# Optimization experiments

Hardware: AMD Instinct MI355X
Metric: run time of the kernel (lower is better)

## Reference

```python
import jax, jax.numpy as jnp
import numpy as np

K_NN = 8        # neighbors
RADIUS = 0.1    # neighbor distance cutoff


def setup_inputs() -> dict:
    key = jax.random.key(0)
    k1, k2 = jax.random.split(key)
    B, N, KS = 2, 8192, 16  # batch, points, mask slots
    pc = jax.random.uniform(k1, (B, N, 3), dtype=jnp.float32)
    mask = jax.random.uniform(k2, (B, N, KS), dtype=jnp.float32)
    return {"pc": pc, "mask": mask}


def _knn(k, pc):
    # squared pairwise distances via gemm: (B,N,N)
    sq = jnp.sum(pc * pc, axis=-1)
    d2 = sq[:, :, None] + sq[:, None, :] - 2.0 * jnp.einsum("bnd,bmd->bnm", pc, pc)
    d2 = jnp.maximum(d2, 0.0)
    neg_d2, idx = jax.lax.top_k(-d2, k)          # k smallest distances
    dist = jnp.sqrt(jnp.maximum(-neg_d2, 0.0))   # (B,N,k) euclidean
    return dist, idx


def reference(pc, mask):
    # mask: (B,N,KS) -> (B,KS,N)
    mask_t = jnp.transpose(mask, (0, 2, 1))
    dist, idx = _knn(K_NN, pc)                   # (B,N,k) each
    # replace out-of-radius neighbors with the self index (nearest = self)
    self_idx = idx[:, :, :1]                     # (B,N,1)
    idx = jnp.where(dist > RADIUS, self_idx, idx)
    idx = jax.lax.stop_gradient(idx)
    # grouping_operation: (B,KS,N) gathered at (B,N,k) -> (B,KS,N,k)
    nn_mask = jax.vmap(lambda f, i: f[:, i])(mask_t, idx)
    # loss_norm=1: L1 norm over mask-slot dim (dim=1), mean over k, mean overall
    diff = mask_t[:, :, :, None] - nn_mask       # (B,KS,N,k)
    loss = jnp.sum(jnp.abs(diff), axis=1).mean(axis=-1)  # (B,N)
    return loss.mean()
```

## Files before the change

kernel.cpp:

```cpp
#include <hip/hip_runtime.h>

#define BATCH 2
#define NPTS  8192
#define KS    16
#define KNN   8
#define R2LOOSE 0.0101f
#define KEYMASK 0xFFFFE000u
#define NCELL   1000
#define CSTRIDE 1024

#define QB       64
#define NWAVE    8
#define NTHREADS 512
#define CAP      32
#define TILEC    1024
#define NBLK     (BATCH * NPTS / QB)

__device__ __forceinline__ int cell_of(float x, float y, float z) {
    int cx = (int)(x * 10.0f); cx = cx > 9 ? 9 : cx;
    int cy = (int)(y * 10.0f); cy = cy > 9 ? 9 : cy;
    int cz = (int)(z * 10.0f); cz = cz > 9 ? 9 : cz;
    return (cx * 10 + cy) * 10 + cz;
}

__global__ __launch_bounds__(1024) void build_kernel(
    const float* __restrict__ pc,
    float4* __restrict__ cs, int* __restrict__ sidx,
    int* __restrict__ cstart, float* __restrict__ out)
{
    __shared__ int h[1024];
    __shared__ int wsum[16];
    const int blk = blockIdx.x, t = threadIdx.x;
    const int b = blk >> 3, seg = blk & 7;
    const int lane = t & 63, w = t >> 6;

    h[t] = 0;
    if (blk == 0 && t == 0) out[0] = 0.0f;

    const float* p = pc + (size_t)b * NPTS * 3;
    float X[8], Y[8], Z[8]; int CC[8];
#pragma unroll
    for (int j = 0; j < 8; ++j) {
        const int i = j * 1024 + t;
        X[j] = p[3 * i]; Y[j] = p[3 * i + 1]; Z[j] = p[3 * i + 2];
        CC[j] = cell_of(X[j], Y[j], Z[j]);
    }
    __syncthreads();

    int myold = 0;
#pragma unroll
    for (int j = 0; j < 8; ++j) {
        const int old = atomicAdd(&h[CC[j]], 1);
        if (j == seg) myold = old;
        __syncthreads();
    }

    const int sum = h[t];
    int inc = sum;
#pragma unroll
    for (int off = 1; off < 64; off <<= 1) {
        const int v = __shfl_up(inc, off);
        if (lane >= off) inc += v;
    }
    if (lane == 63) wsum[w] = inc;
    __syncthreads();
    if (w == 0) {
        const int v = (lane < 16) ? wsum[lane] : 0;
        int iv = v;
#pragma unroll
        for (int off = 1; off < 16; off <<= 1) {
            const int u = __shfl_up(iv, off);
            if (lane >= off) iv += u;
        }
        if (lane < 16) wsum[lane] = iv - v;
    }
    __syncthreads();
    const int excl = inc - sum + wsum[w];
    if (seg == 0) cstart[b * CSTRIDE + t] = excl;
    __syncthreads();
    h[t] = excl;
    __syncthreads();

    float mx = X[0], my_ = Y[0], mz = Z[0]; int mc = CC[0];
#pragma unroll
    for (int j = 1; j < 8; ++j)
        if (seg == j) { mx = X[j]; my_ = Y[j]; mz = Z[j]; mc = CC[j]; }

    const int pos = h[mc] + myold;
    const float sq = fmaf(mz, mz, fmaf(my_, my_, mx * mx));
    cs[b * NPTS + pos]   = make_float4(mx, my_, mz, -0.5f * sq);
    sidx[b * NPTS + pos] = seg * 1024 + t;
}

__global__ __launch_bounds__(512) void knn_loss_kernel(
    const float4* __restrict__ cs,
    const int*    __restrict__ sidx,
    const int*    __restrict__ cstart,
    const float*  __restrict__ mask,
    float* __restrict__ out)
{
    __shared__ float4   tile[TILEC];
    __shared__ int      tsp[TILEC];
    __shared__ unsigned sbuf[CAP * NTHREADS];
    __shared__ int      fidx[QB * KNN];
    __shared__ int      qid[QB];
    __shared__ float    red[NWAVE];

    const int t = threadIdx.x;
    const int q = t & (QB - 1);
    const int s = t >> 6;
    const int su = __builtin_amdgcn_readfirstlane(s);
    const int blk = blockIdx.x;
    const int b  = blk >> 7;
    const int q0 = (blk & 127) * QB;
    const int qpos = q0 + q;

    const float4* csb = cs + b * NPTS;
    const float4 qc = csb[qpos];
    const int    qi = sidx[b * NPTS + qpos];
    if (s == 0) qid[q] = qi;

    const float qx = qc.x, qy = qc.y, qz = qc.z;
    const float qs = -2.0f * qc.w;
    const float negthr = (qs - R2LOOSE) * 0.5f;
    const unsigned SENT = (__float_as_uint(R2LOOSE) & KEYMASK) | 0x1FFFu;

    int lex = cell_of(qx, qy, qz);
    int cmn = lex, cmx = lex;
#pragma unroll
    for (int off = 32; off; off >>= 1) {
        cmn = min(cmn, __shfl_xor(cmn, off));
        cmx = max(cmx, __shfl_xor(cmx, off));
    }
    const int cfirst = __builtin_amdgcn_readfirstlane(cmn);
    const int clast  = __builtin_amdgcn_readfirstlane(cmx);

    int lo0 = cfirst - 111, h0 = clast - 89;
    int lo1 = cfirst - 11,  h1 = clast + 11;
    int lo2 = cfirst + 89,  h2 = clast + 111;
    lo0 = min(max(lo0, 0), 1000);
    lo1 = min(max(lo1, 0), 1000);
    lo2 = min(max(lo2, 0), 1000);
    int hp0 = min(max(h0 + 1, 0), 1000);
    int hp1 = min(max(h1 + 1, 0), 1000);
    int hp2 = min(max(h2 + 1, 0), 1000);
    lo1 = max(lo1, hp0);
    lo2 = max(lo2, hp1);

    const int* csp = cstart + b * CSTRIDE;
    const int P0 = csp[lo0], E0 = csp[hp0];
    const int P1 = csp[lo1], E1 = csp[hp1];
    const int P2 = csp[lo2], E2 = csp[hp2];
    const int L0 = max(0, E0 - P0);
    const int L1 = max(0, E1 - P1);
    const int L2 = max(0, E2 - P2);
    const int C  = L0 + L1 + L2;

    int cnt = 0;
    auto EVAL = [&](const float4& c, int spos) {
        const float tt = fmaf(c.x, qx, fmaf(c.y, qy, fmaf(c.z, qz, c.w)));
        const float d2 = fmaxf(fmaf(-2.0f, tt, qs), 0.0f);
        const unsigned key =
            (__float_as_uint(d2) & KEYMASK) | (unsigned)spos;
        const int slot = cnt < (CAP - 1) ? cnt : (CAP - 1);
        sbuf[slot * NTHREADS + t] = key;
        cnt += (tt >= negthr) ? 1 : 0;
    };

    for (int tb = 0; tb < C; tb += TILEC) {
        const int nt = min(TILEC, C - tb);
        for (int p = t; p < nt; p += NTHREADS) {
            const int g = tb + p;
            int sp = P0 + g;
            sp = (g >= L0)      ? (P1 + (g - L0))      : sp;
            sp = (g >= L0 + L1) ? (P2 + (g - L0 - L1)) : sp;
            tile[p] = csb[sp];
            tsp[p]  = sp;
        }
        __syncthreads();

        int j = (su * nt) >> 3;
        const int e = ((su + 1) * nt) >> 3;
        for (; j + 4 <= e; j += 4) {
            const float4 c0 = tile[j],     c1 = tile[j + 1];
            const float4 c2 = tile[j + 2], c3 = tile[j + 3];
            const int s0 = tsp[j],     s1 = tsp[j + 1];
            const int s2 = tsp[j + 2], s3 = tsp[j + 3];
            EVAL(c0, s0); EVAL(c1, s1); EVAL(c2, s2); EVAL(c3, s3);
        }
        for (; j < e; ++j) { const float4 c0 = tile[j]; EVAL(c0, tsp[j]); }
        __syncthreads();
    }

    unsigned md[KNN];
#pragma unroll
    for (int k = 0; k < KNN; ++k) md[k] = SENT;
    const int m = cnt < CAP ? cnt : CAP;
    for (int k = 0; k < m; ++k) {
        unsigned ky = sbuf[k * NTHREADS + t];
#pragma unroll
        for (int i = 0; i < KNN; ++i) {
            const unsigned mn = min(ky, md[i]);
            const unsigned mx = max(ky, md[i]);
            md[i] = mn; ky = mx;
        }
    }
    __syncthreads();

    {
        uint4* bp = (uint4*)&sbuf[t * KNN];
        bp[0] = make_uint4(md[0], md[1], md[2], md[3]);
        bp[1] = make_uint4(md[4], md[5], md[6], md[7]);
    }
    __syncthreads();

    if (s == 0) {
        for (int l = 1; l < NWAVE; ++l) {
            const uint4* lp = (const uint4*)&sbuf[(l * QB + q) * KNN];
            const uint4 r0 = lp[0], r1 = lp[1];
            const unsigned tk[8] = {r0.x, r0.y, r0.z, r0.w,
                                    r1.x, r1.y, r1.z, r1.w};
#pragma unroll
            for (int k = 0; k < 8; ++k) {
                unsigned ky = tk[k];
                if (ky < md[KNN - 1]) {
#pragma unroll
                    for (int i = 0; i < KNN; ++i) {
                        const unsigned mn = min(ky, md[i]);
                        const unsigned mx = max(ky, md[i]);
                        md[i] = mn; ky = mx;
                    }
                }
            }
        }
#pragma unroll
        for (int k = 0; k < KNN; ++k) {
            const unsigned ky = md[k];
            int nb;
            if (ky >= SENT) {
                nb = qi;
            } else {
                const int sp = (int)(ky & 0x1FFFu);
                const float4 cc = csb[sp];
                const float dx = cc.x - qx;
                const float dy = cc.y - qy;
                const float dz = cc.z - qz;
                const float d2 = fmaf(dx, dx, fmaf(dy, dy, dz * dz));
                nb = (sqrtf(d2) > 0.1f) ? qi : sidx[b * NPTS + sp];
            }
            fidx[q * KNN + k] = nb;
        }
    }
    __syncthreads();

    const int q2 = t >> 3;
    const int j2 = t & 7;
    const int qg = qid[q2];
    const int nb = fidx[q2 * KNN + j2];
    const float* mrow = mask + ((size_t)b * NPTS + qg) * KS;
    const float* nrow = mask + ((size_t)b * NPTS + nb) * KS;
    float acc = 0.0f;
#pragma unroll
    for (int c = 0; c < KS; c += 4) {
        const float4 a = *(const float4*)(mrow + c);
        const float4 v = *(const float4*)(nrow + c);
        acc += fabsf(a.x - v.x) + fabsf(a.y - v.y) +
               fabsf(a.z - v.z) + fabsf(a.w - v.w);
    }

#pragma unroll
    for (int off = 32; off > 0; off >>= 1) acc += __shfl_down(acc, off);
    if ((t & 63) == 0) red[s] = acc;
    __syncthreads();
    if (t == 0) {
        float sum = 0.0f;
#pragma unroll
        for (int i = 0; i < NWAVE; ++i) sum += red[i];
        atomicAdd(out, sum * (1.0f / (BATCH * NPTS * KNN)));
    }
}

extern "C" void kernel_launch(void* const* d_in, const int* in_sizes, int n_in,
                              void* d_out, int out_size, void* d_ws, size_t ws_size,
                              hipStream_t stream) {
    const float* pc   = (const float*)d_in[0];
    const float* mask = (const float*)d_in[1];
    float* out = (float*)d_out;

    float4* cs     = (float4*)d_ws;
    int*    sidx   = (int*)((char*)d_ws + 262144);
    int*    cstart = (int*)((char*)d_ws + 327680);

    hipLaunchKernelGGL(build_kernel, dim3(16), dim3(1024), 0, stream,
                       pc, cs, sidx, cstart, out);
    hipLaunchKernelGGL(knn_loss_kernel, dim3(NBLK), dim3(512), 0, stream,
                       cs, sidx, cstart, mask, out);
}
```

Baseline: 77.40 us.

## Replace LDS candidate tiling with direct wave-uniform global loads

Removes the shared-memory tile staging and its two barriers per tile. Each wave now reads candidate points straight from global memory at wave-uniform addresses, which should turn into scalar or broadcast loads, unrolled eight at a time. The cell-range bounds are made wave-uniform with readfirstlane. This cuts LDS traffic and synchronisation, but now depends on cache hits for the repeated global reads and drops the cooperative coalesced load.

Result: slower. 82.92 us (+7.1%).

```diff
diff --git a/kernel.cpp b/kernel.cpp
--- a/kernel.cpp
+++ b/kernel.cpp
@@ -13,7 +13,6 @@
 #define NWAVE    8
 #define NTHREADS 512
 #define CAP      32
-#define TILEC    1024
 #define NBLK     (BATCH * NPTS / QB)
 
 __device__ __forceinline__ int cell_of(float x, float y, float z) {
@@ -99,8 +98,6 @@
     const float*  __restrict__ mask,
     float* __restrict__ out)
 {
-    __shared__ float4   tile[TILEC];
-    __shared__ int      tsp[TILEC];
     __shared__ unsigned sbuf[CAP * NTHREADS];
     __shared__ int      fidx[QB * KNN];
     __shared__ int      qid[QB];
@@ -148,13 +145,23 @@
     lo2 = max(lo2, hp1);
 
     const int* csp = cstart + b * CSTRIDE;
-    const int P0 = csp[lo0], E0 = csp[hp0];
-    const int P1 = csp[lo1], E1 = csp[hp1];
-    const int P2 = csp[lo2], E2 = csp[hp2];
+    const int P0 = __builtin_amdgcn_readfirstlane(csp[lo0]);
+    const int E0 = __builtin_amdgcn_readfirstlane(csp[hp0]);
+    const int P1 = __builtin_amdgcn_readfirstlane(csp[lo1]);
+    const int E1 = __builtin_amdgcn_readfirstlane(csp[hp1]);
+    const int P2 = __builtin_amdgcn_readfirstlane(csp[lo2]);
+    const int E2 = __builtin_amdgcn_readfirstlane(csp[hp2]);
     const int L0 = max(0, E0 - P0);
     const int L1 = max(0, E1 - P1);
     const int L2 = max(0, E2 - P2);
     const int C  = L0 + L1 + L2;
+
+    auto SPOS = [&](int g) {
+        int sp = P0 + g;
+        sp = (g >= L0)      ? (P1 + (g - L0))      : sp;
+        sp = (g >= L0 + L1) ? (P2 + (g - L0 - L1)) : sp;
+        return sp;
+    };
 
     int cnt = 0;
     auto EVAL = [&](const float4& c, int spos) {
@@ -167,29 +174,24 @@
         cnt += (tt >= negthr) ? 1 : 0;
     };
 
-    for (int tb = 0; tb < C; tb += TILEC) {
-        const int nt = min(TILEC, C - tb);
-        for (int p = t; p < nt; p += NTHREADS) {
-            const int g = tb + p;
-            int sp = P0 + g;
-            sp = (g >= L0)      ? (P1 + (g - L0))      : sp;
-            sp = (g >= L0 + L1) ? (P2 + (g - L0 - L1)) : sp;
-            tile[p] = csb[sp];
-            tsp[p]  = sp;
-        }
-        __syncthreads();
-
-        int j = (su * nt) >> 3;
-        const int e = ((su + 1) * nt) >> 3;
-        for (; j + 4 <= e; j += 4) {
-            const float4 c0 = tile[j],     c1 = tile[j + 1];
-            const float4 c2 = tile[j + 2], c3 = tile[j + 3];
-            const int s0 = tsp[j],     s1 = tsp[j + 1];
-            const int s2 = tsp[j + 2], s3 = tsp[j + 3];
-            EVAL(c0, s0); EVAL(c1, s1); EVAL(c2, s2); EVAL(c3, s3);
-        }
-        for (; j < e; ++j) { const float4 c0 = tile[j]; EVAL(c0, tsp[j]); }
-        __syncthreads();
+    {
+        const int gs = (su * C) >> 3;
+        const int ge = ((su + 1) * C) >> 3;
+        int g = gs;
+        for (; g + 8 <= ge; g += 8) {
+            int sp[8]; float4 c[8];
+#pragma unroll
+            for (int u = 0; u < 8; ++u) sp[u] = SPOS(g + u);
+#pragma unroll
+            for (int u = 0; u < 8; ++u) c[u] = csb[sp[u]];
+#pragma unroll
+            for (int u = 0; u < 8; ++u) EVAL(c[u], sp[u]);
+        }
+        for (; g < ge; ++g) {
+            const int sp = SPOS(g);
+            const float4 c0 = csb[sp];
+            EVAL(c0, sp);
+        }
     }
 
     unsigned md[KNN];
```
